# Performance work log

Hardware: AMD Instinct MI355X
Metric: run time of the kernel (lower is better)

## Reference

```python
import jax, jax.numpy as jnp
import numpy as np

H = 2048
D = 128            # align_dim
TEMP_TAU = 1.0
BIAS_MAX = 0.5
LN_EPS = 1e-5


def _ln(x, g, b):
    m = jnp.mean(x, axis=-1, keepdims=True)
    v = jnp.mean((x - m) ** 2, axis=-1, keepdims=True)
    return (x - m) / jnp.sqrt(v + LN_EPS) * g + b


def _mlp(x, g, b, W1, b1, W2, b2):
    # LayerNorm -> Linear -> GELU(exact) -> Linear
    h = jax.nn.gelu(_ln(x, g, b) @ W1.T + b1, approximate=False)
    return h @ W2.T + b2


def _l2n(x):
    n = jnp.linalg.norm(x, axis=-1, keepdims=True)
    return x / jnp.maximum(n, 1e-12)


def setup_inputs() -> dict:
    key = jax.random.key(0)
    ks = jax.random.split(key, 20)
    B, L = 4096, 4096
    d2 = 2 * D
    s_h = 1.0 / np.sqrt(H)
    s_d2 = 1.0 / np.sqrt(d2)
    inp = {
        "q": jax.random.normal(ks[0], (B, H), jnp.float32),
        "R_non": jax.random.normal(ks[1], (L, H), jnp.float32),
        # mlp_q
        "ln_q_g": jnp.ones((H,), jnp.float32),
        "ln_q_b": jnp.zeros((H,), jnp.float32),
        "W1q": jax.random.uniform(ks[2], (d2, H), jnp.float32, -s_h, s_h),
        "b1q": jnp.zeros((d2,), jnp.float32),
        "W2q": jax.random.uniform(ks[3], (D, d2), jnp.float32, -s_d2, s_d2),
        "b2q": jnp.zeros((D,), jnp.float32),
        # mlp_r
        "ln_r_g": jnp.ones((H,), jnp.float32),
        "ln_r_b": jnp.zeros((H,), jnp.float32),
        "W1r": jax.random.uniform(ks[4], (d2, H), jnp.float32, -s_h, s_h),
        "b1r": jnp.zeros((d2,), jnp.float32),
        "W2r": jax.random.uniform(ks[5], (D, d2), jnp.float32, -s_d2, s_d2),
        "b2r": jnp.zeros((D,), jnp.float32),
        # mlp_dec (input 2D=256 -> 128 -> 1)
        "ln_d_g": jnp.ones((d2,), jnp.float32),
        "ln_d_b": jnp.zeros((d2,), jnp.float32),
        "W1d": jax.random.uniform(ks[6], (128, d2), jnp.float32, -s_d2, s_d2),
        "b1d": jnp.zeros((128,), jnp.float32),
        "W2d": jax.random.uniform(ks[7], (1, 128), jnp.float32, -1 / np.sqrt(128), 1 / np.sqrt(128)),
        "b2d": jnp.zeros((1,), jnp.float32),
        # scalar heads
        "beta": jax.random.uniform(ks[8], (2,), jnp.float32, -0.1, 0.1),
        "W_len": jax.random.uniform(ks[9], (1, 2), jnp.float32, -0.1, 0.1),
        "b_len": jnp.zeros((1,), jnp.float32),
    }
    return inp


def reference(q, R_non, ln_q_g, ln_q_b, W1q, b1q, W2q, b2q,
              ln_r_g, ln_r_b, W1r, b1r, W2r, b2r,
              ln_d_g, ln_d_b, W1d, b1d, W2d, b2d,
              beta, W_len, b_len):
    L = R_non.shape[0]
    z_q = _l2n(_mlp(q, ln_q_g, ln_q_b, W1q, b1q, W2q, b2q))          # [B, D]
    Z_r = _l2n(_mlp(R_non, ln_r_g, ln_r_b, W1r, b1r, W2r, b2r))      # [L, D]
    scores = (z_q @ Z_r.T) / jnp.sqrt(jnp.float32(D))                 # [B, L]
    attn = jax.nn.softmax(scores, axis=-1)                            # [B, L]
    r_bar = _l2n(attn @ Z_r)                                          # [B, D]
    inter = jnp.concatenate([z_q, r_bar], axis=-1)                    # [B, 2D]
    raw_logit = _mlp(inter, ln_d_g, ln_d_b, W1d, b1d, W2d, b2d)[..., 0]  # [B]
    cos_q_r = jnp.sum(z_q * r_bar, axis=-1)                           # [B]
    entropy = -jnp.sum(attn * jnp.log(attn + 1e-8), axis=-1)          # [B]
    u_n = entropy / jnp.log(jnp.float32(L))                           # [B]
    sf = jnp.stack([cos_q_r, u_n], axis=-1)                           # [B, 2]
    delta_len_norm = (sf @ W_len.T + b_len)[..., 0]                   # [B]
    len_feat = jnp.tanh(delta_len_norm / TEMP_TAU)
    delta_theta = jnp.clip(beta[0] * u_n + beta[1] * len_feat, -BIAS_MAX, BIAS_MAX)
    return raw_logit, delta_theta
```

## Files before the change

### kernel.cpp

```cpp
#include <hip/hip_runtime.h>
#include <math.h>


#define HD   2048
#define D2   256
#define DD   128
#define NQ   4096
#define NT   8192
#define NSPLIT 16
#define KPS  (NQ / NSPLIT)
#define NIT  (KPS / 64)

typedef __attribute__((ext_vector_type(8))) short s16x8;
typedef __attribute__((ext_vector_type(4))) float f32x4;

static __device__ __forceinline__ float gelu_exact(float x){
    return 0.5f * x * (1.0f + erff(x * 0.7071067811865475f));
}
static __device__ __forceinline__ unsigned short f2bf(float f){
    unsigned int u = __float_as_uint(f);
    return (unsigned short)((u + 0x7FFFu + ((u >> 16) & 1u)) >> 16);
}
static __device__ __forceinline__ unsigned int pack2bf(float a, float b){
    return (unsigned int)f2bf(a) | ((unsigned int)f2bf(b) << 16);
}

static __device__ __forceinline__ void gload_lds16(const void* g, void* l){
    __builtin_amdgcn_global_load_lds(
        (const __attribute__((address_space(1))) unsigned int*)g,
        (__attribute__((address_space(3))) unsigned int*)l, 16, 0, 0);
}

__global__ __launch_bounds__(256)
void kLN_cast(const float* __restrict__ q, const float* __restrict__ R,
              const float* __restrict__ gq, const float* __restrict__ bq,
              const float* __restrict__ gr, const float* __restrict__ br,
              const float* __restrict__ W1q, const float* __restrict__ W1r,
              unsigned short* __restrict__ Xbf, unsigned short* __restrict__ Wbf){
    const int r = blockIdx.x;
    const int tid = threadIdx.x;
    if (r >= NT){
        const int rw = r - NT;
        const float* src = (rw >= 256) ? (W1r + (size_t)(rw - 256) * HD)
                                       : (W1q + (size_t)rw * HD);
        float4 a = *(const float4*)&src[tid * 8];
        float4 c = *(const float4*)&src[tid * 8 + 4];
        uint4 p = {pack2bf(a.x, a.y), pack2bf(a.z, a.w),
                   pack2bf(c.x, c.y), pack2bf(c.z, c.w)};
        *(uint4*)&Wbf[(size_t)rw * HD + tid * 8] = p;
        return;
    }
    const float* src = (r < NQ) ? (q + (size_t)r * HD) : (R + (size_t)(r - NQ) * HD);
    const float* g  = (r < NQ) ? gq : gr;
    const float* bb = (r < NQ) ? bq : br;
    float4 x0 = *(const float4*)&src[tid * 8];
    float4 x1 = *(const float4*)&src[tid * 8 + 4];
    float v[8] = {x0.x, x0.y, x0.z, x0.w, x1.x, x1.y, x1.z, x1.w};
    float s = 0.f, sq = 0.f;
#pragma unroll
    for (int i = 0; i < 8; ++i){ s += v[i]; sq += v[i] * v[i]; }
    __shared__ float red[256];
    __shared__ float mS, rS;
    red[tid] = s; __syncthreads();
    for (int off = 128; off > 0; off >>= 1){
        if (tid < off) red[tid] += red[tid + off];
        __syncthreads();
    }
    float sum = red[0]; __syncthreads();
    red[tid] = sq; __syncthreads();
    for (int off = 128; off > 0; off >>= 1){
        if (tid < off) red[tid] += red[tid + off];
        __syncthreads();
    }
    if (tid == 0){
        float mean = sum * (1.0f / HD);
        float var  = red[0] * (1.0f / HD) - mean * mean;
        mS = mean;
        rS = rsqrtf(fmaxf(var, 0.0f) + 1e-5f);
    }
    __syncthreads();
    float mean = mS, rstd = rS;
    float4 g0 = *(const float4*)&g[tid * 8];
    float4 g1 = *(const float4*)&g[tid * 8 + 4];
    float4 b0 = *(const float4*)&bb[tid * 8];
    float4 b1 = *(const float4*)&bb[tid * 8 + 4];
    float gg[8] = {g0.x, g0.y, g0.z, g0.w, g1.x, g1.y, g1.z, g1.w};
    float bv[8] = {b0.x, b0.y, b0.z, b0.w, b1.x, b1.y, b1.z, b1.w};
    float h[8];
#pragma unroll
    for (int i = 0; i < 8; ++i) h[i] = (v[i] - mean) * rstd * gg[i] + bv[i];
    uint4 p = {pack2bf(h[0], h[1]), pack2bf(h[2], h[3]),
               pack2bf(h[4], h[5]), pack2bf(h[6], h[7])};
    *(uint4*)&Xbf[(size_t)r * HD + tid * 8] = p;
}

__global__ __launch_bounds__(256)
void k2_mfma(const unsigned short* __restrict__ Xbf,
             const unsigned short* __restrict__ Wbf,
             float* __restrict__ HP){
    const int tid  = threadIdx.x;
    const int wave = tid >> 6, lane = tid & 63;
    const int quad = lane >> 4, col = lane & 15;
    const int mblk = blockIdx.x;
    const int nblk = blockIdx.y;
    const int ks   = blockIdx.z;
    const int inp  = mblk >> 6;
    const int mbase = mblk * 64;
    const int nbase = nblk * 128;
    const int wm = wave & 1, wn = wave >> 1;

    __shared__ __align__(16) char smem[49152];

    const unsigned short* gA[2];
    const unsigned short* gB[4];
#pragma unroll
    for (int i = 0; i < 2; ++i){
        int s = i * 256 + wave * 64 + lane;
        int row = s >> 3, c = (s & 7) ^ (row & 7);
        gA[i] = Xbf + (size_t)(mbase + row) * HD + ks * 1024 + c * 8;
    }
#pragma unroll
    for (int j = 0; j < 4; ++j){
        int s = j * 256 + wave * 64 + lane;
        int row = s >> 3, c = (s & 7) ^ (row & 7);
        gB[j] = Wbf + (size_t)(inp * 256 + nbase + row) * HD + ks * 1024 + c * 8;
    }

#define K2_STAGE(d, k0)                                                        \
    {                                                                          \
        _Pragma("unroll")                                                      \
        for (int i = 0; i < 2; ++i)                                            \
            gload_lds16(gA[i] + (k0),                                          \
                        smem + (d) * 24576 + (i * 256 + wave * 64) * 16);      \
        _Pragma("unroll")                                                      \
        for (int j = 0; j < 4; ++j)                                            \
            gload_lds16(gB[j] + (k0),                                          \
                        smem + (d) * 24576 + 8192 + (j * 256 + wave * 64) * 16);\
    }

    int aoff[2][2], boff[4][2];
#pragma unroll
    for (int mi = 0; mi < 2; ++mi){
        int ra = wm * 32 + mi * 16 + col;
#pragma unroll
        for (int kst = 0; kst < 2; ++kst){
            int cc = kst * 4 + quad;
            aoff[mi][kst] = ra * 128 + ((cc ^ (ra & 7)) << 4);
        }
    }
#pragma unroll
    for (int ni = 0; ni < 4; ++ni){
        int rb = wn * 64 + ni * 16 + col;
#pragma unroll
        for (int kst = 0; kst < 2; ++kst){
            int cc = kst * 4 + quad;
            boff[ni][kst] = rb * 128 + ((cc ^ (rb & 7)) << 4);
        }
    }

    f32x4 acc[2][4];
#pragma unroll
    for (int mi = 0; mi < 2; ++mi)
#pragma unroll
        for (int ni = 0; ni < 4; ++ni) acc[mi][ni] = (f32x4){0.f, 0.f, 0.f, 0.f};

    int cur = 0;
    K2_STAGE(0, 0);
    __syncthreads();
    for (int t = 0; t < 16; ++t){
        if (t < 15) K2_STAGE(cur ^ 1, (t + 1) * 64);
        const char* Ab = smem + cur * 24576;
        const char* Bb = Ab + 8192;
        s16x8 a[2][2], b[4][2];
#pragma unroll
        for (int mi = 0; mi < 2; ++mi)
#pragma unroll
            for (int kst = 0; kst < 2; ++kst)
                a[mi][kst] = *(const s16x8*)(Ab + aoff[mi][kst]);
#pragma unroll
        for (int ni = 0; ni < 4; ++ni)
#pragma unroll
            for (int kst = 0; kst < 2; ++kst)
                b[ni][kst] = *(const s16x8*)(Bb + boff[ni][kst]);
#pragma unroll
        for (int kst = 0; kst < 2; ++kst)
#pragma unroll
            for (int mi = 0; mi < 2; ++mi)
#pragma unroll
                for (int ni = 0; ni < 4; ++ni)
                    acc[mi][ni] = __builtin_amdgcn_mfma_f32_16x16x32_bf16(
                        a[mi][kst], b[ni][kst], acc[mi][ni], 0, 0, 0);
        __syncthreads();
        cur ^= 1;
    }
#undef K2_STAGE

    float* dst = HP + (size_t)ks * NT * D2;
#pragma unroll
    for (int mi = 0; mi < 2; ++mi){
#pragma unroll
        for (int ni = 0; ni < 4; ++ni){
#pragma unroll
            for (int reg = 0; reg < 4; ++reg){
                int m = mbase + wm * 32 + mi * 16 + quad * 4 + reg;
                int n = nbase + wn * 64 + ni * 16 + col;
                dst[(size_t)m * D2 + n] = acc[mi][ni][reg];
            }
        }
    }
}

__global__ __launch_bounds__(256)
void k3_gemm2(const float* __restrict__ HP,
              const float* __restrict__ b1q, const float* __restrict__ b1r,
              const float* __restrict__ W2q, const float* __restrict__ b2q,
              const float* __restrict__ W2r, const float* __restrict__ b2r,
              float* __restrict__ Z, unsigned short* __restrict__ Zbf){
    const int gstart = blockIdx.x * 32;
    const int inp = (gstart >= NQ) ? 1 : 0;
    const float* b1 = inp ? b1r : b1q;
    const float* W2 = inp ? W2r : W2q;
    const float* b2 = inp ? b2r : b2q;

    __shared__ __align__(16) float Hs[32][68];
    __shared__ __align__(16) float Wk[64][132];
    __shared__ float red[32][17];
    __shared__ float normS[32];

    const int tid = threadIdx.x;
    const int ty = tid >> 4;
    const int tx = tid & 15;

    float acc[2][8];
#pragma unroll
    for (int jj = 0; jj < 8; ++jj){ acc[0][jj] = 0.f; acc[1][jj] = 0.f; }

    for (int kc = 0; kc < 4; ++kc){
#pragma unroll
        for (int i = 0; i < 8; ++i){
            int e = tid + i * 256;
            int rr = e >> 6, kk = e & 63;
            size_t idx = (size_t)(gstart + rr) * D2 + kc * 64 + kk;
            float hv = HP[idx] + HP[(size_t)NT * D2 + idx] + b1[kc * 64 + kk];
            Hs[rr][kk] = gelu_exact(hv);
        }
#pragma unroll
        for (int i = 0; i < 32; ++i){
            int e = tid + i * 256;
            int nn = e >> 6, kk = e & 63;
            Wk[kk][nn] = W2[(size_t)nn * D2 + kc * 64 + kk];
        }
        __syncthreads();
#pragma unroll
        for (int k4 = 0; k4 < 16; ++k4){
            float a0[4], a1[4];
            float4 t0 = *(const float4*)&Hs[ty * 2][k4 * 4];
            a0[0] = t0.x; a0[1] = t0.y; a0[2] = t0.z; a0[3] = t0.w;
            float4 t1 = *(const float4*)&Hs[ty * 2 + 1][k4 * 4];
            a1[0] = t1.x; a1[1] = t1.y; a1[2] = t1.z; a1[3] = t1.w;
#pragma unroll
            for (int kq = 0; kq < 4; ++kq){
                float4 w0 = *(const float4*)&Wk[k4 * 4 + kq][tx * 8];
                float4 w1 = *(const float4*)&Wk[k4 * 4 + kq][tx * 8 + 4];
                float wv[8] = {w0.x, w0.y, w0.z, w0.w, w1.x, w1.y, w1.z, w1.w};
#pragma unroll
                for (int jj = 0; jj < 8; ++jj){
                    acc[0][jj] += a0[kq] * wv[jj];
                    acc[1][jj] += a1[kq] * wv[jj];
                }
            }
        }
        __syncthreads();
    }
    float v0[8], v1[8];
    float sq0 = 0.f, sq1 = 0.f;
#pragma unroll
    for (int jj = 0; jj < 8; ++jj){
        int c = tx * 8 + jj;
        v0[jj] = acc[0][jj] + b2[c];
        v1[jj] = acc[1][jj] + b2[c];
        sq0 += v0[jj] * v0[jj];
        sq1 += v1[jj] * v1[jj];
    }
    red[ty * 2][tx]     = sq0;
    red[ty * 2 + 1][tx] = sq1;
    __syncthreads();
    if (tid < 32){
        float s = 0.f;
#pragma unroll
        for (int t = 0; t < 16; ++t) s += red[tid][t];
        normS[tid] = 1.0f / fmaxf(sqrtf(s), 1e-12f);
    }
    __syncthreads();
    float s0 = normS[ty * 2], s1 = normS[ty * 2 + 1];
    int row0 = gstart + ty * 2, row1 = row0 + 1;
    size_t o0 = (size_t)row0 * DD + tx * 8;
    size_t o1 = (size_t)row1 * DD + tx * 8;
    float z0[8], z1[8];
#pragma unroll
    for (int jj = 0; jj < 8; ++jj){ z0[jj] = v0[jj] * s0; z1[jj] = v1[jj] * s1; }
    float4 a = {z0[0], z0[1], z0[2], z0[3]}, b = {z0[4], z0[5], z0[6], z0[7]};
    float4 c = {z1[0], z1[1], z1[2], z1[3]}, d = {z1[4], z1[5], z1[6], z1[7]};
    *(float4*)&Z[o0]     = a;  *(float4*)&Z[o0 + 4] = b;
    *(float4*)&Z[o1]     = c;  *(float4*)&Z[o1 + 4] = d;
    uint4 p0 = {pack2bf(z0[0], z0[1]), pack2bf(z0[2], z0[3]),
                pack2bf(z0[4], z0[5]), pack2bf(z0[6], z0[7])};
    uint4 p1 = {pack2bf(z1[0], z1[1]), pack2bf(z1[2], z1[3]),
                pack2bf(z1[4], z1[5]), pack2bf(z1[6], z1[7])};
    *(uint4*)&Zbf[o0] = p0;
    *(uint4*)&Zbf[o1] = p1;
}

__global__ __launch_bounds__(256)
void kT_transpose(const unsigned short* __restrict__ Zbf,
                  unsigned short* __restrict__ ZbfT){
    __shared__ unsigned short Ts[64][129];
    const int r0 = blockIdx.x * 64;
    const int tid = threadIdx.x;
#pragma unroll
    for (int i = 0; i < 32; ++i){
        int e = tid + i * 256;
        int rr = e >> 7, dd = e & 127;
        Ts[rr][dd] = Zbf[(size_t)(NQ + r0 + rr) * DD + dd];
    }
    __syncthreads();
#pragma unroll
    for (int i = 0; i < 32; ++i){
        int e = tid + i * 256;
        int dd = e >> 6, rr = e & 63;
        ZbfT[(size_t)dd * NQ + r0 + rr] = Ts[rr][dd];
    }
}

__global__ __launch_bounds__(256, 2)
void kA_attn(const unsigned short* __restrict__ Zbf,
             const unsigned short* __restrict__ ZbfT,
             float* __restrict__ OP, float* __restrict__ LW){
    const int tid  = threadIdx.x;
    const int wave = tid >> 6, lane = tid & 63;
    const int quad = lane >> 4, col = lane & 15;
    const int m0   = blockIdx.x * 128 + wave * 32;
    const int split = blockIdx.y;
    const float scl = 0.08838834764831845f;

    __shared__ __align__(16) unsigned short Pt[4][2][16][72];

    s16x8 aq[2][4];
#pragma unroll
    for (int m = 0; m < 2; ++m)
#pragma unroll
        for (int kb = 0; kb < 4; ++kb)
            aq[m][kb] = *(const s16x8*)&Zbf[(size_t)(m0 + m * 16 + col) * DD + kb * 32 + quad * 8];

    f32x4 o[2][8];
#pragma unroll
    for (int m = 0; m < 2; ++m)
#pragma unroll
        for (int dt = 0; dt < 8; ++dt) o[m][dt] = (f32x4){0.f, 0.f, 0.f, 0.f};
    float lp[2][4] = {{0.f,0.f,0.f,0.f},{0.f,0.f,0.f,0.f}};
    float wp[2][4] = {{0.f,0.f,0.f,0.f},{0.f,0.f,0.f,0.f}};

    for (int it = 0; it < NIT; ++it){
        const int r0 = split * KPS + it * 64;

        s16x8 bv[8][2];
#pragma unroll
        for (int dt = 0; dt < 8; ++dt)
#pragma unroll
            for (int kb2 = 0; kb2 < 2; ++kb2)
                bv[dt][kb2] = *(const s16x8*)&ZbfT[(size_t)(dt * 16 + col) * NQ + r0 + kb2 * 32 + quad * 8];

#pragma unroll
        for (int nt = 0; nt < 4; ++nt){
            s16x8 b[4];
#pragma unroll
            for (int kb = 0; kb < 4; ++kb)
                b[kb] = *(const s16x8*)&Zbf[(size_t)(NQ + r0 + nt * 16 + col) * DD + kb * 32 + quad * 8];
#pragma unroll
            for (int m = 0; m < 2; ++m){
                f32x4 s = (f32x4){0.f, 0.f, 0.f, 0.f};
#pragma unroll
                for (int kb = 0; kb < 4; ++kb)
                    s = __builtin_amdgcn_mfma_f32_16x16x32_bf16(aq[m][kb], b[kb], s, 0, 0, 0);
#pragma unroll
                for (int reg = 0; reg < 4; ++reg){
                    float sv = s[reg] * scl;
                    float e  = __expf(sv);
                    lp[m][reg] += e;
                    wp[m][reg] += e * sv;
                    Pt[wave][m][quad * 4 + reg][nt * 16 + col] = f2bf(e);
                }
            }
        }

#pragma unroll
        for (int m = 0; m < 2; ++m){
            s16x8 ap[2];
#pragma unroll
            for (int kb2 = 0; kb2 < 2; ++kb2)
                ap[kb2] = *(const s16x8*)&Pt[wave][m][col][kb2 * 32 + quad * 8];
#pragma unroll
            for (int dt = 0; dt < 8; ++dt)
#pragma unroll
                for (int kb2 = 0; kb2 < 2; ++kb2)
                    o[m][dt] = __builtin_amdgcn_mfma_f32_16x16x32_bf16(ap[kb2], bv[dt][kb2], o[m][dt], 0, 0, 0);
        }
    }

#pragma unroll
    for (int m = 0; m < 2; ++m)
#pragma unroll
    for (int reg = 0; reg < 4; ++reg){
        float l = lp[m][reg], w = wp[m][reg];
        l += __shfl_xor(l, 8);  w += __shfl_xor(w, 8);
        l += __shfl_xor(l, 4);  w += __shfl_xor(w, 4);
        l += __shfl_xor(l, 2);  w += __shfl_xor(w, 2);
        l += __shfl_xor(l, 1);  w += __shfl_xor(w, 1);
        if (col == 0){
            int row = m0 + m * 16 + quad * 4 + reg;
            LW[((size_t)split * NQ + row) * 2]     = l;
            LW[((size_t)split * NQ + row) * 2 + 1] = w;
        }
    }
#pragma unroll
    for (int m = 0; m < 2; ++m)
#pragma unroll
    for (int dt = 0; dt < 8; ++dt){
#pragma unroll
        for (int reg = 0; reg < 4; ++reg){
            int row = m0 + m * 16 + quad * 4 + reg;
            OP[((size_t)split * NQ + row) * DD + dt * 16 + col] = o[m][dt][reg];
        }
    }
}

__global__ __launch_bounds__(128)
void kC_combine(const float* __restrict__ OP, const float* __restrict__ LW,
                const float* __restrict__ Z,
                float* __restrict__ RB, float* __restrict__ COS,
                float* __restrict__ ILW){
    const int r = blockIdx.x;
    const int c = threadIdx.x;
    float v = 0.f;
#pragma unroll
    for (int s = 0; s < NSPLIT; ++s) v += OP[((size_t)s * NQ + r) * DD + c];
    __shared__ float red[128];
    red[c] = v * v; __syncthreads();
    for (int off = 64; off > 0; off >>= 1){
        if (c < off) red[c] += red[c + off];
        __syncthreads();
    }
    float scale = 1.0f / fmaxf(sqrtf(red[0]), 1e-12f);
    __syncthreads();
    float rb = v * scale;
    RB[(size_t)r * DD + c] = rb;
    float zq = Z[(size_t)r * DD + c];
    red[c] = zq * rb; __syncthreads();
    for (int off = 64; off > 0; off >>= 1){
        if (c < off) red[c] += red[c + off];
        __syncthreads();
    }
    if (c == 0){
        COS[r] = red[0];
        float l = 0.f, w = 0.f;
#pragma unroll
        for (int s = 0; s < NSPLIT; ++s){
            l += LW[((size_t)s * NQ + r) * 2];
            w += LW[((size_t)s * NQ + r) * 2 + 1];
        }
        float ent = logf(l) - w / l;
        ILW[2 * r]     = 1.0f / l;
        ILW[2 * r + 1] = ent * (1.0f / 8.317766166719343f);
    }
}

__global__ __launch_bounds__(256)
void k8_decoder(const float* __restrict__ Z, const float* __restrict__ RB,
                const float* __restrict__ ILW, const float* __restrict__ COS,
                const float* __restrict__ gd, const float* __restrict__ bd,
                const float* __restrict__ W1d, const float* __restrict__ b1d,
                const float* __restrict__ W2d, const float* __restrict__ b2d,
                const float* __restrict__ beta, const float* __restrict__ W_len,
                const float* __restrict__ b_len,
                float* __restrict__ out){
    const int r0 = blockIdx.x * 4;
    const int tid = threadIdx.x;
    const int wave = tid >> 6, lane = tid & 63;

    __shared__ __align__(16) float Xs[4][256];
    __shared__ float pr[4][2];

    {
        const int row = r0 + wave;
        const int c0 = lane * 4;
        float4 v;
        if (c0 < DD) v = *(const float4*)&Z[(size_t)row * DD + c0];
        else         v = *(const float4*)&RB[(size_t)row * DD + (c0 - DD)];
        float s  = v.x + v.y + v.z + v.w;
        float sq = v.x * v.x + v.y * v.y + v.z * v.z + v.w * v.w;
#pragma unroll
        for (int off = 32; off > 0; off >>= 1){
            s  += __shfl_xor(s, off);
            sq += __shfl_xor(sq, off);
        }
        float mean = s * (1.0f / D2);
        float var  = sq * (1.0f / D2) - mean * mean;
        float rstd = rsqrtf(fmaxf(var, 0.0f) + 1e-5f);
        float4 g = *(const float4*)&gd[c0];
        float4 b = *(const float4*)&bd[c0];
        float4 xn;
        xn.x = (v.x - mean) * rstd * g.x + b.x;
        xn.y = (v.y - mean) * rstd * g.y + b.y;
        xn.z = (v.z - mean) * rstd * g.z + b.z;
        xn.w = (v.w - mean) * rstd * g.w + b.w;
        *(float4*)&Xs[wave][c0] = xn;
    }
    __syncthreads();

    const int j  = tid & 127;
    const int rp = tid >> 7;
    const float* wrow = W1d + (size_t)j * D2;
    const float* xa = &Xs[rp * 2][0];
    const float* xb = &Xs[rp * 2 + 1][0];
    float h0 = 0.f, h1 = 0.f;
#pragma unroll 8
    for (int k = 0; k < D2; k += 4){
        float4 w  = *(const float4*)&wrow[k];
        float4 a4 = *(const float4*)&xa[k];
        float4 b4 = *(const float4*)&xb[k];
        h0 += w.x * a4.x + w.y * a4.y + w.z * a4.z + w.w * a4.w;
        h1 += w.x * b4.x + w.y * b4.y + w.z * b4.z + w.w * b4.w;
    }
    float bj = b1d[j];
    h0 = gelu_exact(h0 + bj);
    h1 = gelu_exact(h1 + bj);
    float w2 = W2d[j];
    float p0 = h0 * w2, p1 = h1 * w2;
#pragma unroll
    for (int off = 32; off > 0; off >>= 1){
        p0 += __shfl_xor(p0, off);
        p1 += __shfl_xor(p1, off);
    }
    if (lane == 0){ pr[wave][0] = p0; pr[wave][1] = p1; }
    __syncthreads();

    if (tid < 4){
        const int row   = tid;
        const int rpair = row >> 1, rlo = row & 1;
        float lg = b2d[0] + pr[rpair * 2][rlo] + pr[rpair * 2 + 1][rlo];
        const int gr = r0 + row;
        float u  = ILW[2 * gr + 1];
        float cv = COS[gr];
        float dln = cv * W_len[0] + u * W_len[1] + b_len[0];
        float dt = beta[0] * u + beta[1] * tanhf(dln);
        dt = fminf(0.5f, fmaxf(-0.5f, dt));
        out[gr]      = lg;
        out[NQ + gr] = dt;
    }
}

extern "C" void kernel_launch(void* const* d_in, const int* in_sizes, int n_in,
                              void* d_out, int out_size, void* d_ws, size_t ws_size,
                              hipStream_t stream){
    const float* q      = (const float*)d_in[0];
    const float* R      = (const float*)d_in[1];
    const float* ln_q_g = (const float*)d_in[2];
    const float* ln_q_b = (const float*)d_in[3];
    const float* W1q    = (const float*)d_in[4];
    const float* b1q    = (const float*)d_in[5];
    const float* W2q    = (const float*)d_in[6];
    const float* b2q    = (const float*)d_in[7];
    const float* ln_r_g = (const float*)d_in[8];
    const float* ln_r_b = (const float*)d_in[9];
    const float* W1r    = (const float*)d_in[10];
    const float* b1r    = (const float*)d_in[11];
    const float* W2r    = (const float*)d_in[12];
    const float* b2r    = (const float*)d_in[13];
    const float* ln_d_g = (const float*)d_in[14];
    const float* ln_d_b = (const float*)d_in[15];
    const float* W1d    = (const float*)d_in[16];
    const float* b1d    = (const float*)d_in[17];
    const float* W2d    = (const float*)d_in[18];
    const float* b2d    = (const float*)d_in[19];
    const float* beta   = (const float*)d_in[20];
    const float* W_len  = (const float*)d_in[21];
    const float* b_len  = (const float*)d_in[22];

    float* WS = (float*)d_ws;
    unsigned short* Xbf  = (unsigned short*)(WS);
    float* OP    = WS;
    float* HP    = WS + 8388608;
    float* LW    = WS + 8388608;
    unsigned short* Wbf  = (unsigned short*)(WS + 12582912);
    float* Z     = WS + 13107200;
    unsigned short* Zbf  = (unsigned short*)(WS + 14155776);
    unsigned short* ZbfT = (unsigned short*)(WS + 14680064);
    float* RB    = WS + 14942208;
    float* COSV  = WS + 15466496;
    float* ILW   = WS + 15470592;
    float* out   = (float*)d_out;

    hipLaunchKernelGGL(kLN_cast, dim3(NT + 512), dim3(256), 0, stream,
                       q, R, ln_q_g, ln_q_b, ln_r_g, ln_r_b, W1q, W1r, Xbf, Wbf);
    hipLaunchKernelGGL(k2_mfma, dim3(128, 2, 2), dim3(256), 0, stream, Xbf, Wbf, HP);
    hipLaunchKernelGGL(k3_gemm2, dim3(256), dim3(256), 0, stream,
                       HP, b1q, b1r, W2q, b2q, W2r, b2r, Z, Zbf);
    hipLaunchKernelGGL(kT_transpose, dim3(64), dim3(256), 0, stream, Zbf, ZbfT);
    hipLaunchKernelGGL(kA_attn, dim3(32, NSPLIT), dim3(256), 0, stream, Zbf, ZbfT, OP, LW);
    hipLaunchKernelGGL(kC_combine, dim3(NQ), dim3(128), 0, stream, OP, LW, Z, RB, COSV, ILW);
    hipLaunchKernelGGL(k8_decoder, dim3(1024), dim3(256), 0, stream,
                       Z, RB, ILW, COSV, ln_d_g, ln_d_b, W1d, b1d, W2d, b2d,
                       beta, W_len, b_len, out);
}
```

Before: 273.5 us.

## Stage attention K/V tiles in shared LDS via direct global-to-LDS loads

The attention kernel now cooperatively loads each 64-row K tile and the matching transposed V tile into swizzled shared memory with gload_lds16, so all four waves share one copy instead of each wave reading global memory separately. The PV loop is reordered so each V fragment read from LDS feeds both m rows. Two barriers per iteration are added and the occupancy hint of 2 is dropped. The gload_lds16 destination in the GEMM staging macro also gains a per-lane offset, which changes that kernel's addressing.

```diff
diff --git a/kernel.cpp b/kernel.cpp
--- a/kernel.cpp
+++ b/kernel.cpp
@@ -131,11 +131,11 @@
         _Pragma("unroll")                                                      \
         for (int i = 0; i < 2; ++i)                                            \
             gload_lds16(gA[i] + (k0),                                          \
-                        smem + (d) * 24576 + (i * 256 + wave * 64) * 16);      \
+                        smem + (d) * 24576 + (i * 256 + wave * 64 + lane) * 16);\
         _Pragma("unroll")                                                      \
         for (int j = 0; j < 4; ++j)                                            \
             gload_lds16(gB[j] + (k0),                                          \
-                        smem + (d) * 24576 + 8192 + (j * 256 + wave * 64) * 16);\
+                        smem + (d) * 24576 + 8192 + (j * 256 + wave * 64 + lane) * 16);\
     }
 
     int aoff[2][2], boff[4][2];
@@ -332,7 +332,7 @@
     }
 }
 
-__global__ __launch_bounds__(256, 2)
+__global__ __launch_bounds__(256)
 void kA_attn(const unsigned short* __restrict__ Zbf,
              const unsigned short* __restrict__ ZbfT,
              float* __restrict__ OP, float* __restrict__ LW){
@@ -343,6 +343,8 @@
     const int split = blockIdx.y;
     const float scl = 0.08838834764831845f;
 
+    __shared__ __align__(16) char sK[16384];
+    __shared__ __align__(16) char sV[16384];
     __shared__ __align__(16) unsigned short Pt[4][2][16][72];
 
     s16x8 aq[2][4];
@@ -351,6 +353,38 @@
 #pragma unroll
         for (int kb = 0; kb < 4; ++kb)
             aq[m][kb] = *(const s16x8*)&Zbf[(size_t)(m0 + m * 16 + col) * DD + kb * 32 + quad * 8];
+
+    const unsigned short* gK[4];
+    const unsigned short* gV[4];
+    int dK[4], dV[4];
+#pragma unroll
+    for (int i = 0; i < 4; ++i){
+        int s = i * 256 + tid;
+        int row = s >> 4, c = (s & 15) ^ (row & 15);
+        gK[i] = Zbf + (size_t)(NQ + row) * DD + c * 8;
+        dK[i] = s * 16;
+        int s2 = i * 256 + tid;
+        int rv = s2 >> 3, cv = (s2 & 7) ^ (rv & 7);
+        gV[i] = ZbfT + (size_t)rv * NQ + cv * 8;
+        dV[i] = s2 * 16;
+    }
+
+    int kOff[4][4];
+#pragma unroll
+    for (int nt = 0; nt < 4; ++nt){
+        int rb = nt * 16 + col;
+#pragma unroll
+        for (int kb = 0; kb < 4; ++kb)
+            kOff[nt][kb] = rb * 256 + (((kb * 4 + quad) ^ (rb & 15)) << 4);
+    }
+    int vOff[8][2];
+#pragma unroll
+    for (int dt = 0; dt < 8; ++dt){
+        int rv = dt * 16 + col;
+#pragma unroll
+        for (int kb2 = 0; kb2 < 2; ++kb2)
+            vOff[dt][kb2] = rv * 128 + (((kb2 * 4 + quad) ^ (rv & 7)) << 4);
+    }
 
     f32x4 o[2][8];
 #pragma unroll
@@ -362,20 +396,20 @@
 
     for (int it = 0; it < NIT; ++it){
         const int r0 = split * KPS + it * 64;
-
-        s16x8 bv[8][2];
-#pragma unroll
-        for (int dt = 0; dt < 8; ++dt)
-#pragma unroll
-            for (int kb2 = 0; kb2 < 2; ++kb2)
-                bv[dt][kb2] = *(const s16x8*)&ZbfT[(size_t)(dt * 16 + col) * NQ + r0 + kb2 * 32 + quad * 8];
+#pragma unroll
+        for (int i = 0; i < 4; ++i)
+            gload_lds16(gK[i] + (size_t)r0 * DD, sK + dK[i]);
+#pragma unroll
+        for (int i = 0; i < 4; ++i)
+            gload_lds16(gV[i] + r0, sV + dV[i]);
+        __syncthreads();
 
 #pragma unroll
         for (int nt = 0; nt < 4; ++nt){
             s16x8 b[4];
 #pragma unroll
             for (int kb = 0; kb < 4; ++kb)
-                b[kb] = *(const s16x8*)&Zbf[(size_t)(NQ + r0 + nt * 16 + col) * DD + kb * 32 + quad * 8];
+                b[kb] = *(const s16x8*)(sK + kOff[nt][kb]);
 #pragma unroll
             for (int m = 0; m < 2; ++m){
                 f32x4 s = (f32x4){0.f, 0.f, 0.f, 0.f};
@@ -393,18 +427,22 @@
             }
         }
 
-#pragma unroll
-        for (int m = 0; m < 2; ++m){
-            s16x8 ap[2];
+        s16x8 ap[2][2];
+#pragma unroll
+        for (int m = 0; m < 2; ++m)
 #pragma unroll
             for (int kb2 = 0; kb2 < 2; ++kb2)
-                ap[kb2] = *(const s16x8*)&Pt[wave][m][col][kb2 * 32 + quad * 8];
-#pragma unroll
-            for (int dt = 0; dt < 8; ++dt)
-#pragma unroll
-                for (int kb2 = 0; kb2 < 2; ++kb2)
-                    o[m][dt] = __builtin_amdgcn_mfma_f32_16x16x32_bf16(ap[kb2], bv[dt][kb2], o[m][dt], 0, 0, 0);
-        }
+                ap[m][kb2] = *(const s16x8*)&Pt[wave][m][col][kb2 * 32 + quad * 8];
+#pragma unroll
+        for (int dt = 0; dt < 8; ++dt){
+#pragma unroll
+            for (int kb2 = 0; kb2 < 2; ++kb2){
+                s16x8 b = *(const s16x8*)(sV + vOff[dt][kb2]);
+                o[0][dt] = __builtin_amdgcn_mfma_f32_16x16x32_bf16(ap[0][kb2], b, o[0][dt], 0, 0, 0);
+                o[1][dt] = __builtin_amdgcn_mfma_f32_16x16x32_bf16(ap[1][kb2], b, o[1][dt], 0, 0, 0);
+            }
+        }
+        __syncthreads();
     }
 
 #pragma unroll
```

New measurement: 263.6 us. 1.04x faster.
